# Optimization experiments

Measured on AMD Instinct MI355X. Metric: run time of the kernel, lower is better.

## Reference

```python
import jax, jax.numpy as jnp
import numpy as np

N, E, IN, ED, H, G = 30000, 120000, 9, 3, 32, 256


def setup_inputs() -> dict:
    key = jax.random.key(0)
    ks = jax.random.split(key, 20)
    s = 0.1
    inp = {
        "x": jax.random.normal(ks[0], (N, IN), jnp.float32),
        "edge_index": jax.random.randint(ks[1], (2, E), 0, N, jnp.int64),
        "edge_attr": jax.random.normal(ks[2], (E, ED), jnp.float32),
        "batch": jnp.sort(jax.random.randint(ks[3], (N,), 0, G, jnp.int64)),
        # node / edge embeddings
        "Wn": jax.random.normal(ks[4], (IN, H), jnp.float32) * s,
        "bn": jnp.zeros((H,), jnp.float32),
        "We": jax.random.normal(ks[5], (ED, H), jnp.float32) * s,
        "be": jnp.zeros((H,), jnp.float32),
        # 3 NNConv layers stacked on leading axis
        "Wnn": jax.random.normal(ks[6], (3, H, H * H), jnp.float32) * s,
        "bnn": jnp.zeros((3, H * H), jnp.float32),
        "Wroot": jax.random.normal(ks[7], (3, H, H), jnp.float32) * s,
        "bconv": jnp.zeros((3, H), jnp.float32),
        # MLP head
        "W1": jax.random.normal(ks[8], (H, 128), jnp.float32) * s,
        "b1": jnp.zeros((128,), jnp.float32),
        "W2": jax.random.normal(ks[9], (128, 64), jnp.float32) * s,
        "b2": jnp.zeros((64,), jnp.float32),
        "W3": jax.random.normal(ks[10], (64, 1), jnp.float32) * s,
        "b3": jnp.zeros((1,), jnp.float32),
    }
    return inp


def reference(x, edge_index, edge_attr, batch, Wn, bn, We, be, Wnn, bnn, Wroot, bconv, W1, b1, W2, b2, W3, b3):
    relu = jax.nn.relu
    h = relu(x @ Wn + bn)                      # [N, H]
    ea = relu(edge_attr @ We + be)             # [E, H]
    src, dst = edge_index[0], edge_index[1]

    def nnconv(hin, k):
        # edge-conditioned weight matrices: [E, H, H] (in, out)
        Wmat = (ea @ Wnn[k] + bnn[k]).reshape(-1, H, H)
        msg = jnp.einsum('ei,eio->eo', hin[src], Wmat)          # per-edge matvec
        agg = jax.ops.segment_sum(msg, dst, num_segments=N)     # scatter-add
        return agg + hin @ Wroot[k] + bconv[k]                  # root weight + bias

    x1 = relu(nnconv(h, 0)); s1 = x1 + h
    x2 = relu(nnconv(s1, 1)); s2 = x2 + s1
    x3 = relu(nnconv(s2, 2)); s3 = x3 + s2

    pooled = jax.ops.segment_sum(s3, batch, num_segments=G)     # global_add_pool [G, H]
    out = relu(pooled @ W1 + b1)
    out = relu(out @ W2 + b2)
    return out @ W3 + b3                                        # [G, 1]
```

## Files before the change

kernel.cpp:

```cpp
#include <hip/hip_runtime.h>
#include <hip/hip_bf16.h>
#include <hip/hip_fp16.h>

#define N_NODES 30000
#define N_EDGES 120000
#define IN_DIM  9
#define H       32
#define G_GRAPHS 256
#define NSTEP   66

#define ZERO_FLOATS  ((3 * N_NODES * H) / 2 + G_GRAPHS * H)
#define ZERO_BLOCKS  ((ZERO_FLOATS + 255) / 256)
#define EMBED_BLOCKS 3750
#define WCONV_BLOCKS 396

typedef __attribute__((ext_vector_type(2)))  __fp16 half2v;
typedef __attribute__((ext_vector_type(8)))  __fp16 half8v;
typedef __attribute__((ext_vector_type(16))) float f32x16;

__global__ __launch_bounds__(256) void prologue_k(
    float* __restrict__ zbase, const float* __restrict__ x,
    const float* __restrict__ Wn, const float* __restrict__ bn,
    __fp16* __restrict__ s, const float* __restrict__ Wnn,
    const float* __restrict__ bnn, __fp16* __restrict__ wf)
{
    const int b = blockIdx.x;
    if (b < ZERO_BLOCKS) {
        int i = b * 256 + threadIdx.x;
        if (i < ZERO_FLOATS) zbase[i] = 0.f;
    } else if (b < ZERO_BLOCKS + EMBED_BLOCKS) {
        int gid = (b - ZERO_BLOCKS) * 256 + threadIdx.x;
        int n = gid >> 5, o = gid & 31;
        float acc = bn[o];
        #pragma unroll
        for (int i = 0; i < IN_DIM; ++i)
            acc = fmaf(x[n * IN_DIM + i], Wn[i * H + o], acc);
        s[gid] = (__fp16)fmaxf(acc, 0.f);
    } else {
        int gid = (b - ZERO_BLOCKS - EMBED_BLOCKS) * 256 + threadIdx.x;
        int layer = gid / (NSTEP * 512);
        int rem   = gid % (NSTEP * 512);
        int step  = rem >> 9;
        int lane  = (rem >> 3) & 63;
        int t     = gid & 7;
        int krow  = step * 16 + ((lane >> 5) << 3) + t;
        int col   = lane & 31;
        float v = (krow < 1024) ? Wnn[layer * 32768 + krow * 32 + col]
                                : bnn[layer * 1024 + (krow - 1024) * 32 + col];
        wf[gid] = (__fp16)v;
    }
}

__global__ __launch_bounds__(64) void edge_mfma_k(
    const __fp16* __restrict__ s, const float* __restrict__ eattr,
    const int* __restrict__ ei, const float* __restrict__ We,
    const float* __restrict__ be, const __fp16* __restrict__ wf,
    __fp16* __restrict__ agg)
{
    const int lane = threadIdx.x;
    const int ebase = blockIdx.x * 64;
    const int er = lane & 31;
    const int hi = lane >> 5;

    const int e0 = ebase + er;
    const int e1 = ebase + 32 + er;

    const float a00 = eattr[e0*3+0], a01 = eattr[e0*3+1], a02 = eattr[e0*3+2];
    const float a10 = eattr[e1*3+0], a11 = eattr[e1*3+1], a12 = eattr[e1*3+2];

    const int src0 = ei[e0], src1 = ei[e1];

    const half8v h0lo = *(const half8v*)(s + src0 * H + hi * 8);
    const half8v h0hi = *(const half8v*)(s + src0 * H + 16 + hi * 8);
    const half8v h1lo = *(const half8v*)(s + src1 * H + hi * 8);
    const half8v h1hi = *(const half8v*)(s + src1 * H + 16 + hi * 8);

    f32x16 acc0 = {};
    f32x16 acc1 = {};
    half2v ea0 = {(__fp16)1.f, (__fp16)1.f};
    half2v ea1 = ea0;

    #pragma unroll
    for (int step = 0; step < NSTEP; ++step) {
        const int j = step >> 1;
        if ((step & 1) == 0 && j < 32) {
            const float w0 = We[j], w1 = We[32+j], w2 = We[64+j], bb = be[j];
            float f0 = fmaxf(fmaf(a02, w2, fmaf(a01, w1, fmaf(a00, w0, bb))), 0.f);
            float f1 = fmaxf(fmaf(a12, w2, fmaf(a11, w1, fmaf(a10, w0, bb))), 0.f);
            ea0 = __builtin_amdgcn_cvt_pkrtz(f0, f0);
            ea1 = __builtin_amdgcn_cvt_pkrtz(f1, f1);
        }
        const half8v c0 = (step & 1) ? h0hi : h0lo;
        const half8v c1 = (step & 1) ? h1hi : h1lo;
        half8v A0, A1;
        if (j < 32) {
            #pragma unroll
            for (int q = 0; q < 4; ++q) {
                half2v p0 = { c0[2*q], c0[2*q+1] };
                half2v p1 = { c1[2*q], c1[2*q+1] };
                half2v m0 = ea0 * p0;
                half2v m1 = ea1 * p1;
                A0[2*q] = m0[0]; A0[2*q+1] = m0[1];
                A1[2*q] = m1[0]; A1[2*q+1] = m1[1];
            }
        } else {
            A0 = c0; A1 = c1;
        }
        const half8v B = *(const half8v*)(wf + ((step * 64 + lane) << 3));
        acc0 = __builtin_amdgcn_mfma_f32_32x32x16_f16(A0, B, acc0, 0, 0, 0);
        acc1 = __builtin_amdgcn_mfma_f32_32x32x16_f16(A1, B, acc1, 0, 0, 0);
    }

    const int* dsts = ei + N_EDGES;
    const int o = er;
    #pragma unroll
    for (int reg = 0; reg < 16; ++reg) {
        const int r = (reg & 3) + 8 * (reg >> 2) + 4 * hi;
        const int d0 = dsts[ebase + r];
        const int d1 = dsts[ebase + 32 + r];
        float v0 = acc0[reg], v1 = acc1[reg];
        float q0 = __shfl_xor(v0, 1);
        float q1 = __shfl_xor(v1, 1);
        if ((er & 1) == 0) {
            half2v p0 = __builtin_amdgcn_cvt_pkrtz(v0, q0);
            half2v p1 = __builtin_amdgcn_cvt_pkrtz(v1, q1);
            __half2 u0, u1;
            __builtin_memcpy(&u0, &p0, 4);
            __builtin_memcpy(&u1, &p1, 4);
            unsafeAtomicAdd((__half2*)(agg + d0 * H + o), u0);
            unsafeAtomicAdd((__half2*)(agg + d1 * H + o), u1);
        }
    }
}

__global__ __launch_bounds__(256) void finalize_k(
    const __fp16* __restrict__ agg, const __fp16* __restrict__ sin,
    const float* __restrict__ Wroot, const float* __restrict__ bconv,
    __fp16* __restrict__ sout, const int* __restrict__ batch,
    float* __restrict__ pooled, int do_pool)
{
    int gid = blockIdx.x * 256 + threadIdx.x;
    if (gid >= N_NODES * H) return;
    int n = gid >> 5, o = gid & 31;
    float acc = bconv[o];
    const __fp16* row = sin + n * H;
    #pragma unroll
    for (int i = 0; i < H; ++i)
        acc = fmaf((float)row[i], Wroot[i * H + o], acc);
    float val = fmaxf((float)agg[gid] + acc, 0.f) + (float)sin[gid];
    if (do_pool) {
        const int lane = threadIdx.x & 63;
        const int b = batch[n];
        const float ov = __shfl_down(val, 32);
        const int   ob = __shfl_down(b, 32);
        const int   ub = __shfl_up(b, 32);
        if (lane < 32) {
            float v = (ob == b) ? val + ov : val;
            atomicAdd(pooled + b * H + o, v);
        } else if (ub != b) {
            atomicAdd(pooled + b * H + o, val);
        }
    } else {
        sout[gid] = (__fp16)val;
    }
}

__global__ __launch_bounds__(128) void mlp_k(
    const float* __restrict__ pooled,
    const float* __restrict__ W1, const float* __restrict__ b1,
    const float* __restrict__ W2, const float* __restrict__ b2,
    const float* __restrict__ W3, const float* __restrict__ b3,
    float* __restrict__ out)
{
    __shared__ float p[H];
    __shared__ float h1[128];
    __shared__ float h2[64];
    const int g = blockIdx.x, t = threadIdx.x;
    if (t < H) p[t] = pooled[g * H + t];
    __syncthreads();
    float a = b1[t];
    #pragma unroll
    for (int i = 0; i < H; ++i)
        a = fmaf(p[i], W1[i * 128 + t], a);
    h1[t] = fmaxf(a, 0.f);
    __syncthreads();
    if (t < 64) {
        float a2 = b2[t];
        #pragma unroll 4
        for (int i = 0; i < 128; ++i)
            a2 = fmaf(h1[i], W2[i * 64 + t], a2);
        h2[t] = fmaxf(a2, 0.f);
    }
    __syncthreads();
    if (t < 64) {
        float v = h2[t] * W3[t];
        #pragma unroll
        for (int off = 32; off > 0; off >>= 1)
            v += __shfl_down(v, off);
        if (t == 0) out[g] = v + b3[0];
    }
}

extern "C" void kernel_launch(void* const* d_in, const int* in_sizes, int n_in,
                              void* d_out, int out_size, void* d_ws, size_t ws_size,
                              hipStream_t stream)
{
    const float* x     = (const float*)d_in[0];
    const int*   ei    = (const int*)  d_in[1];
    const float* eattr = (const float*)d_in[2];
    const int*   batch = (const int*)  d_in[3];
    const float* Wn    = (const float*)d_in[4];
    const float* bn    = (const float*)d_in[5];
    const float* We    = (const float*)d_in[6];
    const float* be    = (const float*)d_in[7];
    const float* Wnn   = (const float*)d_in[8];
    const float* bnn   = (const float*)d_in[9];
    const float* Wroot = (const float*)d_in[10];
    const float* bconv = (const float*)d_in[11];
    const float* W1    = (const float*)d_in[12];
    const float* b1    = (const float*)d_in[13];
    const float* W2    = (const float*)d_in[14];
    const float* b2    = (const float*)d_in[15];
    const float* W3    = (const float*)d_in[16];
    const float* b3    = (const float*)d_in[17];
    float* out = (float*)d_out;

    __fp16* agg0  = (__fp16*)d_ws;
    __fp16* agg1  = agg0 + N_NODES * H;
    __fp16* agg2  = agg1 + N_NODES * H;
    float* pooled = (float*)(agg2 + N_NODES * H);
    __fp16* s0    = (__fp16*)(pooled + G_GRAPHS * H);
    __fp16* s1    = s0 + N_NODES * H;
    __fp16* wf    = s1 + N_NODES * H;
    __fp16* aggs[3] = {agg0, agg1, agg2};

    const int nw_grid = (N_NODES * H + 255) / 256;
    const int e_grid  = N_EDGES / 64;

    prologue_k<<<ZERO_BLOCKS + EMBED_BLOCKS + WCONV_BLOCKS, 256, 0, stream>>>(
        (float*)d_ws, x, Wn, bn, s0, Wnn, bnn, wf);

    const __fp16* sin = s0;
    __fp16* sout = s1;
    for (int k = 0; k < 3; ++k) {
        edge_mfma_k<<<e_grid, 64, 0, stream>>>(sin, eattr, ei, We, be,
                                               wf + k * NSTEP * 512, aggs[k]);
        finalize_k<<<nw_grid, 256, 0, stream>>>(aggs[k], sin,
                                                Wroot + k * H * H,
                                                bconv + k * H, sout,
                                                batch, pooled, (k == 2) ? 1 : 0);
        const __fp16* tmp = sout; sout = (__fp16*)sin; sin = tmp;
    }

    mlp_k<<<G_GRAPHS, 128, 0, stream>>>(pooled, W1, b1, W2, b2, W3, b3, out);
}
```

Measured before the change: 105.2 us.

## Vectorize root matmul with fp16 dot2, fuse agg zeroing into finalize, shuffle dst indices

Pre-transposes Wroot to fp16 in the prologue so finalize can use vectorized half8 loads and fdot2 instead of 32 scalar fp32 loads per output. Zeroing of the next layer's aggregation buffer moves from the prologue into the previous finalize pass, which shrinks the prologue's zero region. The edge kernel loads destination indices once per lane and broadcasts them with shuffles rather than doing 32 scalar global loads per lane. The root matmul now uses fp16 weights, which costs some precision.

```diff
diff --git a/kernel.cpp b/kernel.cpp
--- a/kernel.cpp
+++ b/kernel.cpp
@@ -9,10 +9,11 @@
 #define G_GRAPHS 256
 #define NSTEP   66
 
-#define ZERO_FLOATS  ((3 * N_NODES * H) / 2 + G_GRAPHS * H)
-#define ZERO_BLOCKS  ((ZERO_FLOATS + 255) / 256)
+#define ZERO_FLOATS  ((N_NODES * H) / 2 + G_GRAPHS * H)
+#define ZERO_BLOCKS  (ZERO_FLOATS / 256)
 #define EMBED_BLOCKS 3750
 #define WCONV_BLOCKS 396
+#define WRT_BLOCKS   12
 
 typedef __attribute__((ext_vector_type(2)))  __fp16 half2v;
 typedef __attribute__((ext_vector_type(8)))  __fp16 half8v;
@@ -22,12 +23,13 @@
     float* __restrict__ zbase, const float* __restrict__ x,
     const float* __restrict__ Wn, const float* __restrict__ bn,
     __fp16* __restrict__ s, const float* __restrict__ Wnn,
-    const float* __restrict__ bnn, __fp16* __restrict__ wf)
+    const float* __restrict__ bnn, __fp16* __restrict__ wf,
+    const float* __restrict__ Wroot, __fp16* __restrict__ wrT)
 {
     const int b = blockIdx.x;
     if (b < ZERO_BLOCKS) {
         int i = b * 256 + threadIdx.x;
-        if (i < ZERO_FLOATS) zbase[i] = 0.f;
+        zbase[i] = 0.f;
     } else if (b < ZERO_BLOCKS + EMBED_BLOCKS) {
         int gid = (b - ZERO_BLOCKS) * 256 + threadIdx.x;
         int n = gid >> 5, o = gid & 31;
@@ -36,7 +38,7 @@
         for (int i = 0; i < IN_DIM; ++i)
             acc = fmaf(x[n * IN_DIM + i], Wn[i * H + o], acc);
         s[gid] = (__fp16)fmaxf(acc, 0.f);
-    } else {
+    } else if (b < ZERO_BLOCKS + EMBED_BLOCKS + WCONV_BLOCKS) {
         int gid = (b - ZERO_BLOCKS - EMBED_BLOCKS) * 256 + threadIdx.x;
         int layer = gid / (NSTEP * 512);
         int rem   = gid % (NSTEP * 512);
@@ -48,6 +50,13 @@
         float v = (krow < 1024) ? Wnn[layer * 32768 + krow * 32 + col]
                                 : bnn[layer * 1024 + (krow - 1024) * 32 + col];
         wf[gid] = (__fp16)v;
+    } else {
+        int gid = (b - ZERO_BLOCKS - EMBED_BLOCKS - WCONV_BLOCKS) * 256
+                  + threadIdx.x;
+        int layer = gid >> 10;
+        int rem   = gid & 1023;
+        int o = rem >> 5, i = rem & 31;
+        wrT[gid] = (__fp16)Wroot[layer * 1024 + i * 32 + o];
     }
 }
 
@@ -64,6 +73,8 @@
 
     const int e0 = ebase + er;
     const int e1 = ebase + 32 + er;
+
+    const int dst_l = ei[N_EDGES + ebase + lane];
 
     const float a00 = eattr[e0*3+0], a01 = eattr[e0*3+1], a02 = eattr[e0*3+2];
     const float a10 = eattr[e1*3+0], a11 = eattr[e1*3+1], a12 = eattr[e1*3+2];
@@ -111,13 +122,12 @@
         acc1 = __builtin_amdgcn_mfma_f32_32x32x16_f16(A1, B, acc1, 0, 0, 0);
     }
 
-    const int* dsts = ei + N_EDGES;
     const int o = er;
     #pragma unroll
     for (int reg = 0; reg < 16; ++reg) {
         const int r = (reg & 3) + 8 * (reg >> 2) + 4 * hi;
-        const int d0 = dsts[ebase + r];
-        const int d1 = dsts[ebase + 32 + r];
+        const int d0 = __shfl(dst_l, r);
+        const int d1 = __shfl(dst_l, 32 + r);
         float v0 = acc0[reg], v1 = acc1[reg];
         float q0 = __shfl_xor(v0, 1);
         float q1 = __shfl_xor(v1, 1);
@@ -135,18 +145,27 @@
 
 __global__ __launch_bounds__(256) void finalize_k(
     const __fp16* __restrict__ agg, const __fp16* __restrict__ sin,
-    const float* __restrict__ Wroot, const float* __restrict__ bconv,
-    __fp16* __restrict__ sout, const int* __restrict__ batch,
-    float* __restrict__ pooled, int do_pool)
+    const __fp16* __restrict__ wrT, const float* __restrict__ bconv,
+    __fp16* __restrict__ sout, __fp16* __restrict__ aggnext,
+    const int* __restrict__ batch, float* __restrict__ pooled, int do_pool)
 {
     int gid = blockIdx.x * 256 + threadIdx.x;
     if (gid >= N_NODES * H) return;
     int n = gid >> 5, o = gid & 31;
     float acc = bconv[o];
-    const __fp16* row = sin + n * H;
-    #pragma unroll
-    for (int i = 0; i < H; ++i)
-        acc = fmaf((float)row[i], Wroot[i * H + o], acc);
+    const half8v* rowv = (const half8v*)(sin + n * H);
+    const half8v* wrv  = (const half8v*)(wrT + o * H);
+    #pragma unroll
+    for (int q = 0; q < 4; ++q) {
+        half8v r8 = rowv[q];
+        half8v w8 = wrv[q];
+        #pragma unroll
+        for (int p = 0; p < 4; ++p) {
+            half2v rp = { r8[2*p], r8[2*p+1] };
+            half2v wp = { w8[2*p], w8[2*p+1] };
+            acc = __builtin_amdgcn_fdot2(rp, wp, acc, false);
+        }
+    }
     float val = fmaxf((float)agg[gid] + acc, 0.f) + (float)sin[gid];
     if (do_pool) {
         const int lane = threadIdx.x & 63;
@@ -162,6 +181,7 @@
         }
     } else {
         sout[gid] = (__fp16)val;
+        aggnext[gid] = (__fp16)0.f;
     }
 }
 
@@ -226,19 +246,21 @@
     float* out = (float*)d_out;
 
     __fp16* agg0  = (__fp16*)d_ws;
-    __fp16* agg1  = agg0 + N_NODES * H;
+    float* pooled = (float*)(agg0 + N_NODES * H);
+    __fp16* agg1  = (__fp16*)(pooled + G_GRAPHS * H);
     __fp16* agg2  = agg1 + N_NODES * H;
-    float* pooled = (float*)(agg2 + N_NODES * H);
-    __fp16* s0    = (__fp16*)(pooled + G_GRAPHS * H);
+    __fp16* s0    = agg2 + N_NODES * H;
     __fp16* s1    = s0 + N_NODES * H;
     __fp16* wf    = s1 + N_NODES * H;
-    __fp16* aggs[3] = {agg0, agg1, agg2};
+    __fp16* wrT   = wf + 3 * NSTEP * 512;
+    __fp16* aggs[4] = {agg0, agg1, agg2, agg0};
 
     const int nw_grid = (N_NODES * H + 255) / 256;
     const int e_grid  = N_EDGES / 64;
 
-    prologue_k<<<ZERO_BLOCKS + EMBED_BLOCKS + WCONV_BLOCKS, 256, 0, stream>>>(
-        (float*)d_ws, x, Wn, bn, s0, Wnn, bnn, wf);
+    prologue_k<<<ZERO_BLOCKS + EMBED_BLOCKS + WCONV_BLOCKS + WRT_BLOCKS,
+                 256, 0, stream>>>(
+        (float*)d_ws, x, Wn, bn, s0, Wnn, bnn, wf, Wroot, wrT);
 
     const __fp16* sin = s0;
     __fp16* sout = s1;
@@ -246,8 +268,9 @@
         edge_mfma_k<<<e_grid, 64, 0, stream>>>(sin, eattr, ei, We, be,
                                                wf + k * NSTEP * 512, aggs[k]);
         finalize_k<<<nw_grid, 256, 0, stream>>>(aggs[k], sin,
-                                                Wroot + k * H * H,
+                                                wrT + k * 1024,
                                                 bconv + k * H, sout,
+                                                aggs[k + 1],
                                                 batch, pooled, (k == 2) ? 1 : 0);
         const __fp16* tmp = sout; sout = (__fp16*)sin; sin = tmp;
     }
```

Result: faster. 95.45 us, median of 3 (-9.3%).
